# Kernel optimization log

Hardware: AMD Instinct MI355X
Metric: run time of the kernel (lower is better)

## Reference

```python
import jax, jax.numpy as jnp
import numpy as np

N_NODES = 50000
N_REL = 16
N_BASIS = 8
D_IN = 64
D_HID = 64
N_CLASS = 16
N_EDGES = 800000


def setup_inputs() -> dict:
    key = jax.random.key(0)
    ks = jax.random.split(key, 9)
    x = jax.random.normal(ks[0], (N_NODES, D_IN), dtype=jnp.float32)
    edge_index = jax.random.randint(ks[1], (2, N_EDGES), 0, N_NODES, dtype=jnp.int64)
    edge_type = jax.random.randint(ks[2], (N_EDGES,), 0, N_REL, dtype=jnp.int64)
    s1 = 1.0 / np.sqrt(D_IN)
    s2 = 1.0 / np.sqrt(D_HID)
    # layer 1: basis decomposition W_r = sum_b coeffs[r,b] * bases[b]
    bases1 = jax.random.normal(ks[3], (N_BASIS, D_IN, D_HID), dtype=jnp.float32) * s1
    coeffs1 = jax.random.normal(ks[4], (N_REL, N_BASIS), dtype=jnp.float32)
    self1 = jax.random.normal(ks[5], (D_IN, D_HID), dtype=jnp.float32) * s1
    # layer 2
    bases2 = jax.random.normal(ks[6], (N_BASIS, D_HID, N_CLASS), dtype=jnp.float32) * s2
    coeffs2 = jax.random.normal(ks[7], (N_REL, N_BASIS), dtype=jnp.float32)
    self2 = jax.random.normal(ks[8], (D_HID, N_CLASS), dtype=jnp.float32) * s2
    return {"x": x, "bases1": bases1, "coeffs1": coeffs1, "self1": self1,
            "bases2": bases2, "coeffs2": coeffs2, "self2": self2,
            "edge_index": edge_index, "edge_type": edge_type}


def _rgcn_layer(h, bases, coeffs, self_w, src, seg_id, inv_c):
    # normalized messages gathered from source nodes: [E, d]
    msg = h[src] * inv_c[:, None]
    # fused per-(relation, target-node) segment reduce -> [R, N, d]
    agg = jax.ops.segment_sum(msg, seg_id, num_segments=N_REL * N_NODES)
    agg = agg.reshape(N_REL, N_NODES, -1)
    # per-relation weights from basis decomposition: [R, d_in, d_out]
    w_rel = jnp.einsum('rb,bio->rio', coeffs, bases)
    return jnp.einsum('rni,rio->no', agg, w_rel) + h @ self_w


def reference(x, bases1, coeffs1, self1, bases2, coeffs2, self2, edge_index, edge_type):
    src, dst = edge_index[0], edge_index[1]
    # normalization constants: per-relation in-degree of each target node
    counts = jnp.zeros((N_REL, N_NODES), dtype=jnp.float32).at[edge_type, dst].add(1.0)
    inv_c = 1.0 / jnp.maximum(counts[edge_type, dst], 1.0)  # [E]
    seg_id = edge_type * N_NODES + dst  # combined (relation, node) segment key
    h = jax.nn.relu(_rgcn_layer(x, bases1, coeffs1, self1, src, seg_id, inv_c))
    logits = _rgcn_layer(h, bases2, coeffs2, self2, src, seg_id, inv_c)
    return logits
```

## Files before the change

### kernel.cpp

```cpp
#include <hip/hip_runtime.h>

#define N_NODES 50000
#define N_REL 16
#define N_BASIS 8
#define D_IN 64
#define D_HID 64
#define N_CLASS 16
#define N_EDGES 800000
#define N_SBLK 196
#define G1_BLOCKS 782
#define CNT_BLOCKS 3125
#define WREL_BLOCKS 340

typedef short s8v __attribute__((ext_vector_type(8)));
typedef float f4v __attribute__((ext_vector_type(4)));

__device__ inline unsigned short f2bf(float f) {
    union { float f; unsigned u; } v; v.f = f;
    unsigned r = (v.u + 0x7FFFu + ((v.u >> 16) & 1u)) >> 16;
    return (unsigned short)r;
}
__device__ inline float bf2f(unsigned short b) {
    union { unsigned u; float f; } v; v.u = ((unsigned)b) << 16;
    return v.f;
}

__global__ __launch_bounds__(256) void k_pre(const float* __restrict__ b1, const float* __restrict__ c1,
                                             const float* __restrict__ s1f,
                                             const float* __restrict__ b2, const float* __restrict__ c2,
                                             const float* __restrict__ s2f,
                                             unsigned short* __restrict__ w1T,
                                             unsigned short* __restrict__ w2T,
                                             const int* __restrict__ ei,
                                             const int* __restrict__ et,
                                             int* __restrict__ counts) {
    if (blockIdx.x >= WREL_BLOCKS) {
        int e = (blockIdx.x - WREL_BLOCKS) * 256 + threadIdx.x;
        if (e < N_EDGES) {
            int dst = ei[N_EDGES + e];
            int t = et[e];
            atomicAdd(&counts[dst * 16 + t], 1);
        }
        return;
    }
    int idx = blockIdx.x * 256 + threadIdx.x;
    if (idx < 17 * 4096) {
        int r = idx >> 12;
        int o = (idx >> 6) & 63;
        int k = idx & 63;
        float acc = 0.f;
        if (r < 16) {
            #pragma unroll
            for (int b = 0; b < N_BASIS; b++) acc += c1[r * N_BASIS + b] * b1[b * 4096 + k * 64 + o];
        } else {
            acc = s1f[k * 64 + o];
        }
        w1T[idx] = f2bf(acc);
    } else {
        int idx2 = idx - 17 * 4096;
        if (idx2 < 17 * 1024) {
            int r = idx2 >> 10;
            int o = (idx2 >> 6) & 15;
            int k = idx2 & 63;
            float acc = 0.f;
            if (r < 16) {
                #pragma unroll
                for (int b = 0; b < N_BASIS; b++) acc += c2[r * N_BASIS + b] * b2[b * 1024 + k * 16 + o];
            } else {
                acc = s2f[k * 16 + o];
            }
            w2T[idx2] = f2bf(acc);
        }
    }
}

__global__ __launch_bounds__(256) void k_scan_local(const int* __restrict__ counts,
                                                    int* __restrict__ offsets,
                                                    int* __restrict__ bsum) {
    __shared__ int s[256];
    int t = threadIdx.x;
    int i = blockIdx.x * 256 + t;
    int v = 0;
    if (i < N_NODES) {
        const int4* c4 = (const int4*)(counts + i * 16);
        #pragma unroll
        for (int j = 0; j < 4; j++) {
            int4 cv = c4[j];
            v += cv.x + cv.y + cv.z + cv.w;
        }
    }
    s[t] = v;
    __syncthreads();
    #pragma unroll
    for (int off = 1; off < 256; off <<= 1) {
        int x = (t >= off) ? s[t - off] : 0;
        __syncthreads();
        s[t] += x;
        __syncthreads();
    }
    if (i < N_NODES) offsets[i] = s[t] - v;
    if (t == 255) bsum[blockIdx.x] = s[255];
}

__global__ __launch_bounds__(256) void k_scan_bsum(int* __restrict__ bsum) {
    __shared__ int s[256];
    int t = threadIdx.x;
    int v = (t < N_SBLK) ? bsum[t] : 0;
    s[t] = v;
    __syncthreads();
    #pragma unroll
    for (int off = 1; off < 256; off <<= 1) {
        int x = (t >= off) ? s[t - off] : 0;
        __syncthreads();
        s[t] += x;
        __syncthreads();
    }
    if (t < N_SBLK) bsum[t] = s[t] - v;
}

__global__ __launch_bounds__(256) void k_scan_final(int* __restrict__ offsets,
                                                    const int* __restrict__ bsum,
                                                    int* __restrict__ cursor) {
    int i = blockIdx.x * 256 + threadIdx.x;
    if (i < N_NODES) {
        int o = offsets[i] + bsum[blockIdx.x];
        offsets[i] = o;
        cursor[i] = o;
    }
    if (i == 0) offsets[N_NODES] = N_EDGES;
}

__global__ __launch_bounds__(256) void k_fused1(const float* __restrict__ x,
                                                const unsigned short* __restrict__ w1T,
                                                unsigned short* __restrict__ t1,
                                                unsigned short* __restrict__ h,
                                                const int* __restrict__ ei,
                                                const int* __restrict__ et,
                                                const int* __restrict__ counts,
                                                int* __restrict__ cursor,
                                                int2* __restrict__ sed) {
    if (blockIdx.x >= G1_BLOCKS) {
        int e = (blockIdx.x - G1_BLOCKS) * 256 + threadIdx.x;
        if (e < N_EDGES) {
            int src = ei[e];
            int dst = ei[N_EDGES + e];
            int t = et[e];
            int pos = atomicAdd(&cursor[dst], 1);
            float inv = 1.0f / (float)counts[dst * 16 + t];
            sed[pos] = make_int2((t << 16) | src, __float_as_int(inv));
        }
        return;
    }
    __shared__ __align__(16) unsigned short wbuf[2][64 * 64];
    __shared__ __align__(16) unsigned short ou[4][16 * 64];
    int tid = threadIdx.x;
    int wv = tid >> 6, lane = tid & 63;
    int m = lane & 15, q = lane >> 4;
    int nb = blockIdx.x * 64 + wv * 16;
    bool active = (nb < N_NODES);
    int n = active ? (nb + m) : 0;

    const float* xr = x + (size_t)n * 64 + q * 8;
    float4 x0a = *(const float4*)(xr);
    float4 x0b = *(const float4*)(xr + 4);
    float4 x1a = *(const float4*)(xr + 32);
    float4 x1b = *(const float4*)(xr + 36);
    s8v b0, b1;
    b0[0] = f2bf(x0a.x); b0[1] = f2bf(x0a.y); b0[2] = f2bf(x0a.z); b0[3] = f2bf(x0a.w);
    b0[4] = f2bf(x0b.x); b0[5] = f2bf(x0b.y); b0[6] = f2bf(x0b.z); b0[7] = f2bf(x0b.w);
    b1[0] = f2bf(x1a.x); b1[1] = f2bf(x1a.y); b1[2] = f2bf(x1a.z); b1[3] = f2bf(x1a.w);
    b1[4] = f2bf(x1b.x); b1[5] = f2bf(x1b.y); b1[6] = f2bf(x1b.z); b1[7] = f2bf(x1b.w);

    int c0 = tid, c1 = tid + 256;
    int p0s = (c0 >> 3) * 64 + (((c0 & 7) ^ ((c0 >> 3) & 7)) << 3);
    int p1s = (c1 >> 3) * 64 + (((c1 & 7) ^ ((c1 >> 3) & 7)) << 3);

    {
        const int4* src = (const int4*)w1T;
        int4 v0 = src[c0], v1 = src[c1];
        *(int4*)&wbuf[0][p0s] = v0;
        *(int4*)&wbuf[0][p1s] = v1;
    }
    __syncthreads();

    for (int w = 0; w < 17; w++) {
        int cur = w & 1;
        if (w < 16) {
            const int4* src = (const int4*)w1T + (w + 1) * 512;
            int4 v0 = src[c0], v1 = src[c1];
            *(int4*)&wbuf[cur ^ 1][p0s] = v0;
            *(int4*)&wbuf[cur ^ 1][p1s] = v1;
        }
        #pragma unroll
        for (int ct = 0; ct < 4; ct++) {
            int ro = ct * 16 + m;
            int pa = q ^ (ro & 7);
            int pb = (4 + q) ^ (ro & 7);
            s8v A0 = *(const s8v*)&wbuf[cur][ro * 64 + pa * 8];
            s8v A1 = *(const s8v*)&wbuf[cur][ro * 64 + pb * 8];
            f4v acc = (f4v){0.f, 0.f, 0.f, 0.f};
            acc = __builtin_amdgcn_mfma_f32_16x16x32_bf16(A0, b0, acc, 0, 0, 0);
            acc = __builtin_amdgcn_mfma_f32_16x16x32_bf16(A1, b1, acc, 0, 0, 0);
            ushort4 o4;
            o4.x = f2bf(acc[0]); o4.y = f2bf(acc[1]); o4.z = f2bf(acc[2]); o4.w = f2bf(acc[3]);
            int g = ct * 2 + (q >> 1);
            int pg = g ^ (m & 7);
            *(ushort4*)&ou[wv][m * 64 + pg * 8 + (q & 1) * 4] = o4;
        }
        if (active) {
            int r1 = lane >> 3, g1 = lane & 7;
            int pg1 = g1 ^ (r1 & 7);
            int4 d0 = *(const int4*)&ou[wv][r1 * 64 + pg1 * 8];
            int4 d1 = *(const int4*)&ou[wv][(r1 + 8) * 64 + pg1 * 8];
            unsigned short* base = (w < 16) ? (t1 + ((size_t)w * N_NODES + nb) * 64)
                                            : (h + (size_t)nb * 64);
            *(int4*)(base + lane * 8) = d0;
            *(int4*)(base + 512 + lane * 8) = d1;
        }
        __syncthreads();
    }
}

__global__ __launch_bounds__(256) void k_agg1(const int* __restrict__ offsets,
                                              const int2* __restrict__ sed,
                                              const unsigned short* __restrict__ t1,
                                              unsigned short* __restrict__ h) {
    int tid = threadIdx.x;
    int n = blockIdx.x * 4 + (tid >> 6);
    int lane = tid & 63;
    int slot = lane >> 3;
    int d8 = lane & 7;
    int start = offsets[n];
    int end = offsets[n + 1];
    float a[8];
    #pragma unroll
    for (int j = 0; j < 8; j++) a[j] = 0.f;
    for (int i = start + slot; i < end; i += 16) {
        int2 e0 = sed[i];
        bool has1 = (i + 8) < end;
        int2 e1 = has1 ? sed[i + 8] : e0;
        float inv0 = __int_as_float(e0.y);
        float inv1 = has1 ? __int_as_float(e1.y) : 0.f;
        int id0 = e0.x, id1 = e1.x;
        const unsigned short* r0 = t1 + ((size_t)((id0 >> 16) * N_NODES + (id0 & 0xFFFF))) * 64 + d8 * 8;
        const unsigned short* r1 = t1 + ((size_t)((id1 >> 16) * N_NODES + (id1 & 0xFFFF))) * 64 + d8 * 8;
        ushort4 v00 = *(const ushort4*)(r0);
        ushort4 v01 = *(const ushort4*)(r0 + 4);
        ushort4 v10 = *(const ushort4*)(r1);
        ushort4 v11 = *(const ushort4*)(r1 + 4);
        a[0] += inv0 * bf2f(v00.x); a[1] += inv0 * bf2f(v00.y);
        a[2] += inv0 * bf2f(v00.z); a[3] += inv0 * bf2f(v00.w);
        a[4] += inv0 * bf2f(v01.x); a[5] += inv0 * bf2f(v01.y);
        a[6] += inv0 * bf2f(v01.z); a[7] += inv0 * bf2f(v01.w);
        a[0] += inv1 * bf2f(v10.x); a[1] += inv1 * bf2f(v10.y);
        a[2] += inv1 * bf2f(v10.z); a[3] += inv1 * bf2f(v10.w);
        a[4] += inv1 * bf2f(v11.x); a[5] += inv1 * bf2f(v11.y);
        a[6] += inv1 * bf2f(v11.z); a[7] += inv1 * bf2f(v11.w);
    }
    #pragma unroll
    for (int j = 0; j < 8; j++) {
        a[j] += __shfl_xor(a[j], 8, 64);
        a[j] += __shfl_xor(a[j], 16, 64);
        a[j] += __shfl_xor(a[j], 32, 64);
    }
    if (slot == 0) {
        size_t hi = (size_t)n * 64 + d8 * 8;
        ushort4 h0 = *(const ushort4*)(h + hi);
        ushort4 h1 = *(const ushort4*)(h + hi + 4);
        ushort4 o0, o1;
        o0.x = f2bf(bf2f(h0.x) + a[0]); o0.y = f2bf(bf2f(h0.y) + a[1]);
        o0.z = f2bf(bf2f(h0.z) + a[2]); o0.w = f2bf(bf2f(h0.w) + a[3]);
        o1.x = f2bf(bf2f(h1.x) + a[4]); o1.y = f2bf(bf2f(h1.y) + a[5]);
        o1.z = f2bf(bf2f(h1.z) + a[6]); o1.w = f2bf(bf2f(h1.w) + a[7]);
        *(ushort4*)(h + hi) = o0;
        *(ushort4*)(h + hi + 4) = o1;
    }
}

__global__ __launch_bounds__(256) void k_gemm2(const unsigned short* __restrict__ h,
                                               const unsigned short* __restrict__ w2T,
                                               unsigned short* __restrict__ t2, float* __restrict__ out) {
    __shared__ __align__(16) unsigned short wall[272 * 64];
    int tid = threadIdx.x;
    int wv = tid >> 6, lane = tid & 63;
    int m = lane & 15, q = lane >> 4;
    int nb = blockIdx.x * 64 + wv * 16;

    for (int c = tid; c < 2176; c += 256) {
        int4 v = ((const int4*)w2T)[c];
        int row = c >> 3, g = c & 7;
        *(int4*)&wall[row * 64 + ((g ^ (row & 7)) << 3)] = v;
    }
    __syncthreads();
    if (nb >= N_NODES) return;
    int n = nb + m;

    s8v b0 = *(const s8v*)(h + (size_t)n * 64 + q * 8);
    s8v b1 = *(const s8v*)(h + (size_t)n * 64 + 32 + q * 8);
    #pragma unroll
    for (int j = 0; j < 8; j++) {
        if ((unsigned short)b0[j] & 0x8000u) b0[j] = 0;
        if ((unsigned short)b1[j] & 0x8000u) b1[j] = 0;
    }

    for (int w = 0; w < 17; w++) {
        int ro = w * 16 + m;
        int pa = q ^ (ro & 7);
        int pb = (4 + q) ^ (ro & 7);
        s8v A0 = *(const s8v*)&wall[ro * 64 + pa * 8];
        s8v A1 = *(const s8v*)&wall[ro * 64 + pb * 8];
        f4v acc = (f4v){0.f, 0.f, 0.f, 0.f};
        acc = __builtin_amdgcn_mfma_f32_16x16x32_bf16(A0, b0, acc, 0, 0, 0);
        acc = __builtin_amdgcn_mfma_f32_16x16x32_bf16(A1, b1, acc, 0, 0, 0);
        if (w < 16) {
            ushort4 o;
            o.x = f2bf(acc[0]); o.y = f2bf(acc[1]); o.z = f2bf(acc[2]); o.w = f2bf(acc[3]);
            *(ushort4*)(t2 + ((size_t)w * N_NODES + n) * 16 + q * 4) = o;
        } else {
            *(float4*)(out + (size_t)n * 16 + q * 4) = make_float4(acc[0], acc[1], acc[2], acc[3]);
        }
    }
}

__global__ __launch_bounds__(256) void k_agg2(const int* __restrict__ offsets,
                                              const int2* __restrict__ sed,
                                              const unsigned short* __restrict__ t2,
                                              float* __restrict__ out) {
    int tid = threadIdx.x;
    int n = blockIdx.x * 16 + (tid >> 4);
    int sub = tid & 15;
    int slot = sub >> 1;
    int d2 = sub & 1;
    int start = offsets[n];
    int end = offsets[n + 1];
    float a[8];
    #pragma unroll
    for (int j = 0; j < 8; j++) a[j] = 0.f;
    for (int i = start + slot; i < end; i += 16) {
        int2 e0 = sed[i];
        bool has1 = (i + 8) < end;
        int2 e1 = has1 ? sed[i + 8] : e0;
        float inv0 = __int_as_float(e0.y);
        float inv1 = has1 ? __int_as_float(e1.y) : 0.f;
        int id0 = e0.x, id1 = e1.x;
        const unsigned short* r0 = t2 + ((size_t)((id0 >> 16) * N_NODES + (id0 & 0xFFFF))) * 16 + d2 * 8;
        const unsigned short* r1 = t2 + ((size_t)((id1 >> 16) * N_NODES + (id1 & 0xFFFF))) * 16 + d2 * 8;
        ushort4 v00 = *(const ushort4*)(r0);
        ushort4 v01 = *(const ushort4*)(r0 + 4);
        ushort4 v10 = *(const ushort4*)(r1);
        ushort4 v11 = *(const ushort4*)(r1 + 4);
        a[0] += inv0 * bf2f(v00.x); a[1] += inv0 * bf2f(v00.y);
        a[2] += inv0 * bf2f(v00.z); a[3] += inv0 * bf2f(v00.w);
        a[4] += inv0 * bf2f(v01.x); a[5] += inv0 * bf2f(v01.y);
        a[6] += inv0 * bf2f(v01.z); a[7] += inv0 * bf2f(v01.w);
        a[0] += inv1 * bf2f(v10.x); a[1] += inv1 * bf2f(v10.y);
        a[2] += inv1 * bf2f(v10.z); a[3] += inv1 * bf2f(v10.w);
        a[4] += inv1 * bf2f(v11.x); a[5] += inv1 * bf2f(v11.y);
        a[6] += inv1 * bf2f(v11.z); a[7] += inv1 * bf2f(v11.w);
    }
    #pragma unroll
    for (int j = 0; j < 8; j++) {
        a[j] += __shfl_xor(a[j], 2, 64);
        a[j] += __shfl_xor(a[j], 4, 64);
        a[j] += __shfl_xor(a[j], 8, 64);
    }
    if (slot == 0) {
        float* p = out + (size_t)n * 16 + d2 * 8;
        float4 c0 = *(const float4*)p;
        float4 c1 = *(const float4*)(p + 4);
        c0.x += a[0]; c0.y += a[1]; c0.z += a[2]; c0.w += a[3];
        c1.x += a[4]; c1.y += a[5]; c1.z += a[6]; c1.w += a[7];
        *(float4*)p = c0;
        *(float4*)(p + 4) = c1;
    }
}

extern "C" void kernel_launch(void* const* d_in, const int* in_sizes, int n_in,
                              void* d_out, int out_size, void* d_ws, size_t ws_size,
                              hipStream_t stream) {
    const float* x      = (const float*)d_in[0];
    const float* bases1 = (const float*)d_in[1];
    const float* coeffs1= (const float*)d_in[2];
    const float* self1  = (const float*)d_in[3];
    const float* bases2 = (const float*)d_in[4];
    const float* coeffs2= (const float*)d_in[5];
    const float* self2  = (const float*)d_in[6];
    const int*   ei     = (const int*)d_in[7];
    const int*   et     = (const int*)d_in[8];
    float* out = (float*)d_out;

    char* ws = (char*)d_ws;
    int*            counts  = (int*)(ws + 0);
    int*            offsets = (int*)(ws + 3200000);
    int*            cursor  = (int*)(ws + 3400064);
    unsigned short* w1T     = (unsigned short*)(ws + 3600128);
    unsigned short* w2T     = (unsigned short*)(ws + 3739392);
    int*            bsum    = (int*)(ws + 3774208);
    int2*           sed     = (int2*)(ws + 3775232);
    unsigned short* h       = (unsigned short*)(ws + 10175232);
    unsigned short* t1      = (unsigned short*)(ws + 16575232);
    unsigned short* t2      = t1;

    hipMemsetAsync(counts, 0, 3200000, stream);
    k_pre<<<WREL_BLOCKS + CNT_BLOCKS, 256, 0, stream>>>(
        bases1, coeffs1, self1, bases2, coeffs2, self2, w1T, w2T, ei, et, counts);
    k_scan_local<<<N_SBLK, 256, 0, stream>>>(counts, offsets, bsum);
    k_scan_bsum<<<1, 256, 0, stream>>>(bsum);
    k_scan_final<<<N_SBLK, 256, 0, stream>>>(offsets, bsum, cursor);
    k_fused1<<<G1_BLOCKS + CNT_BLOCKS, 256, 0, stream>>>(x, w1T, t1, h, ei, et, counts, cursor, sed);
    k_agg1<<<12500, 256, 0, stream>>>(offsets, sed, t1, h);
    k_gemm2<<<(N_NODES + 63) / 64, 256, 0, stream>>>(h, w2T, t2, out);
    k_agg2<<<3125, 256, 0, stream>>>(offsets, sed, t2, out);
}
```

Before: 222.2 us.

## Fuse layer-1 aggregation with layer-2 GEMM and split GEMM1 across count/scatter kernels

Splits the layer-1 node-transform GEMM into two halves, running one half alongside edge counting and the other alongside the CSR scatter, so both atomic passes overlap tensor work. Layer-1 aggregation is fused with ReLU and the layer-2 MFMA GEMM in one kernel, which removes the intermediate write and reread of h and one launch. Aggregation now uses one lane group per node with 16B loads instead of slot-parallel shuffle reductions. In exchange, each node's edges are walked serially by a single thread, so high-degree nodes can cause load imbalance, and t2 gets its own buffer instead of reusing t1.

```diff
diff --git a/kernel.cpp b/kernel.cpp
--- a/kernel.cpp
+++ b/kernel.cpp
@@ -8,9 +8,8 @@
 #define N_CLASS 16
 #define N_EDGES 800000
 #define N_SBLK 196
-#define G1_BLOCKS 782
+#define G1H_BLOCKS 391
 #define CNT_BLOCKS 3125
-#define WREL_BLOCKS 340
 
 typedef short s8v __attribute__((ext_vector_type(8)));
 typedef float f4v __attribute__((ext_vector_type(4)));
@@ -24,30 +23,26 @@
     union { unsigned u; float f; } v; v.u = ((unsigned)b) << 16;
     return v.f;
 }
-
-__global__ __launch_bounds__(256) void k_pre(const float* __restrict__ b1, const float* __restrict__ c1,
-                                             const float* __restrict__ s1f,
-                                             const float* __restrict__ b2, const float* __restrict__ c2,
-                                             const float* __restrict__ s2f,
-                                             unsigned short* __restrict__ w1T,
-                                             unsigned short* __restrict__ w2T,
-                                             const int* __restrict__ ei,
-                                             const int* __restrict__ et,
-                                             int* __restrict__ counts) {
-    if (blockIdx.x >= WREL_BLOCKS) {
-        int e = (blockIdx.x - WREL_BLOCKS) * 256 + threadIdx.x;
-        if (e < N_EDGES) {
-            int dst = ei[N_EDGES + e];
-            int t = et[e];
-            atomicAdd(&counts[dst * 16 + t], 1);
-        }
-        return;
-    }
+__device__ __forceinline__ void acc8(float* a, float inv, int4 p) {
+    a[0] += inv * __int_as_float((int)((unsigned)p.x << 16));
+    a[1] += inv * __int_as_float(p.x & (int)0xFFFF0000u);
+    a[2] += inv * __int_as_float((int)((unsigned)p.y << 16));
+    a[3] += inv * __int_as_float(p.y & (int)0xFFFF0000u);
+    a[4] += inv * __int_as_float((int)((unsigned)p.z << 16));
+    a[5] += inv * __int_as_float(p.z & (int)0xFFFF0000u);
+    a[6] += inv * __int_as_float((int)((unsigned)p.w << 16));
+    a[7] += inv * __int_as_float(p.w & (int)0xFFFF0000u);
+}
+
+__global__ __launch_bounds__(256) void k_wrel(const float* __restrict__ b1, const float* __restrict__ c1,
+                                              const float* __restrict__ s1f,
+                                              const float* __restrict__ b2, const float* __restrict__ c2,
+                                              const float* __restrict__ s2f,
+                                              unsigned short* __restrict__ w1T,
+                                              unsigned short* __restrict__ w2T) {
     int idx = blockIdx.x * 256 + threadIdx.x;
     if (idx < 17 * 4096) {
-        int r = idx >> 12;
-        int o = (idx >> 6) & 63;
-        int k = idx & 63;
+        int r = idx >> 12, o = (idx >> 6) & 63, k = idx & 63;
         float acc = 0.f;
         if (r < 16) {
             #pragma unroll
@@ -59,9 +54,7 @@
     } else {
         int idx2 = idx - 17 * 4096;
         if (idx2 < 17 * 1024) {
-            int r = idx2 >> 10;
-            int o = (idx2 >> 6) & 15;
-            int k = idx2 & 63;
+            int r = idx2 >> 10, o = (idx2 >> 6) & 15, k = idx2 & 63;
             float acc = 0.f;
             if (r < 16) {
                 #pragma unroll
@@ -72,6 +65,127 @@
             w2T[idx2] = f2bf(acc);
         }
     }
+}
+
+__device__ __forceinline__ void gemm1_tile(int tile, int tid,
+                                           const float* __restrict__ x,
+                                           const unsigned short* __restrict__ w1T,
+                                           unsigned short* __restrict__ t1,
+                                           unsigned short* __restrict__ h,
+                                           unsigned short* wbuf,
+                                           unsigned short* ou) {
+    int wv = tid >> 6, lane = tid & 63;
+    int m = lane & 15, q = lane >> 4;
+    int nb = tile * 64 + wv * 16;
+    bool active = (nb < N_NODES);
+    int n = active ? (nb + m) : 0;
+
+    const float* xr = x + (size_t)n * 64 + q * 8;
+    float4 x0a = *(const float4*)(xr);
+    float4 x0b = *(const float4*)(xr + 4);
+    float4 x1a = *(const float4*)(xr + 32);
+    float4 x1b = *(const float4*)(xr + 36);
+    s8v b0, b1;
+    b0[0] = f2bf(x0a.x); b0[1] = f2bf(x0a.y); b0[2] = f2bf(x0a.z); b0[3] = f2bf(x0a.w);
+    b0[4] = f2bf(x0b.x); b0[5] = f2bf(x0b.y); b0[6] = f2bf(x0b.z); b0[7] = f2bf(x0b.w);
+    b1[0] = f2bf(x1a.x); b1[1] = f2bf(x1a.y); b1[2] = f2bf(x1a.z); b1[3] = f2bf(x1a.w);
+    b1[4] = f2bf(x1b.x); b1[5] = f2bf(x1b.y); b1[6] = f2bf(x1b.z); b1[7] = f2bf(x1b.w);
+
+    int c0 = tid, c1 = tid + 256;
+    int p0s = (c0 >> 3) * 64 + (((c0 & 7) ^ ((c0 >> 3) & 7)) << 3);
+    int p1s = (c1 >> 3) * 64 + (((c1 & 7) ^ ((c1 >> 3) & 7)) << 3);
+
+    {
+        const int4* src = (const int4*)w1T;
+        int4 v0 = src[c0], v1 = src[c1];
+        *(int4*)&wbuf[p0s] = v0;
+        *(int4*)&wbuf[p1s] = v1;
+    }
+    __syncthreads();
+
+    for (int w = 0; w < 17; w++) {
+        int cur = w & 1;
+        if (w < 16) {
+            const int4* src = (const int4*)w1T + (w + 1) * 512;
+            int4 v0 = src[c0], v1 = src[c1];
+            *(int4*)&wbuf[(cur ^ 1) * 4096 + p0s] = v0;
+            *(int4*)&wbuf[(cur ^ 1) * 4096 + p1s] = v1;
+        }
+        #pragma unroll
+        for (int ct = 0; ct < 4; ct++) {
+            int ro = ct * 16 + m;
+            int pa = q ^ (ro & 7);
+            int pb = (4 + q) ^ (ro & 7);
+            s8v A0 = *(const s8v*)&wbuf[cur * 4096 + ro * 64 + pa * 8];
+            s8v A1 = *(const s8v*)&wbuf[cur * 4096 + ro * 64 + pb * 8];
+            f4v acc = (f4v){0.f, 0.f, 0.f, 0.f};
+            acc = __builtin_amdgcn_mfma_f32_16x16x32_bf16(A0, b0, acc, 0, 0, 0);
+            acc = __builtin_amdgcn_mfma_f32_16x16x32_bf16(A1, b1, acc, 0, 0, 0);
+            ushort4 o4;
+            o4.x = f2bf(acc[0]); o4.y = f2bf(acc[1]); o4.z = f2bf(acc[2]); o4.w = f2bf(acc[3]);
+            int g = ct * 2 + (q >> 1);
+            int pg = g ^ (m & 7);
+            *(ushort4*)&ou[wv * 1024 + m * 64 + pg * 8 + (q & 1) * 4] = o4;
+        }
+        if (active) {
+            int r1 = lane >> 3, g1 = lane & 7;
+            int pg1 = g1 ^ (r1 & 7);
+            int4 d0 = *(const int4*)&ou[wv * 1024 + r1 * 64 + pg1 * 8];
+            int4 d1 = *(const int4*)&ou[wv * 1024 + (r1 + 8) * 64 + pg1 * 8];
+            unsigned short* base = (w < 16) ? (t1 + ((size_t)w * N_NODES + nb) * 64)
+                                            : (h + (size_t)nb * 64);
+            *(int4*)(base + lane * 8) = d0;
+            *(int4*)(base + 512 + lane * 8) = d1;
+        }
+        __syncthreads();
+    }
+}
+
+__global__ __launch_bounds__(256) void k_fusedA(const float* __restrict__ x,
+                                                const unsigned short* __restrict__ w1T,
+                                                unsigned short* __restrict__ t1,
+                                                unsigned short* __restrict__ h,
+                                                const int* __restrict__ ei,
+                                                const int* __restrict__ et,
+                                                int* __restrict__ counts) {
+    __shared__ __align__(16) unsigned short wbuf[2 * 4096];
+    __shared__ __align__(16) unsigned short ou[4 * 1024];
+    if (blockIdx.x >= G1H_BLOCKS) {
+        int e = (blockIdx.x - G1H_BLOCKS) * 256 + threadIdx.x;
+        if (e < N_EDGES) {
+            int dst = ei[N_EDGES + e];
+            int t = et[e];
+            atomicAdd(&counts[dst * 16 + t], 1);
+        }
+        return;
+    }
+    gemm1_tile(blockIdx.x, threadIdx.x, x, w1T, t1, h, wbuf, ou);
+}
+
+__global__ __launch_bounds__(256) void k_fusedB(const float* __restrict__ x,
+                                                const unsigned short* __restrict__ w1T,
+                                                unsigned short* __restrict__ t1,
+                                                unsigned short* __restrict__ h,
+                                                const int* __restrict__ ei,
+                                                const int* __restrict__ et,
+                                                const int* __restrict__ counts,
+                                                int* __restrict__ cursor,
+                                                int2* __restrict__ sed) {
+    __shared__ __align__(16) unsigned short wbuf[2 * 4096];
+    __shared__ __align__(16) unsigned short ou[4 * 1024];
+    if (blockIdx.x >= G1H_BLOCKS) {
+        int e = (blockIdx.x - G1H_BLOCKS) * 256 + threadIdx.x;
+        if (e < N_EDGES) {
+            int src = ei[e];
+            int dst = ei[N_EDGES + e];
+            int t = et[e];
+            int pos = atomicAdd(&cursor[dst], 1);
+            float inv = 1.0f / (float)counts[dst * 16 + t];
+            sed[pos] = make_int2((t << 16) | src, __float_as_int(inv));
+        }
+        return;
+    }
+    gemm1_tile(blockIdx.x + G1H_BLOCKS, threadIdx.x, x, w1T, t1, h, wbuf, ou);
 }
 
 __global__ __launch_bounds__(256) void k_scan_local(const int* __restrict__ counts,
@@ -130,194 +244,76 @@
     if (i == 0) offsets[N_NODES] = N_EDGES;
 }
 
-__global__ __launch_bounds__(256) void k_fused1(const float* __restrict__ x,
-                                                const unsigned short* __restrict__ w1T,
-                                                unsigned short* __restrict__ t1,
-                                                unsigned short* __restrict__ h,
-                                                const int* __restrict__ ei,
-                                                const int* __restrict__ et,
-                                                const int* __restrict__ counts,
-                                                int* __restrict__ cursor,
-                                                int2* __restrict__ sed) {
-    if (blockIdx.x >= G1_BLOCKS) {
-        int e = (blockIdx.x - G1_BLOCKS) * 256 + threadIdx.x;
-        if (e < N_EDGES) {
-            int src = ei[e];
-            int dst = ei[N_EDGES + e];
-            int t = et[e];
-            int pos = atomicAdd(&cursor[dst], 1);
-            float inv = 1.0f / (float)counts[dst * 16 + t];
-            sed[pos] = make_int2((t << 16) | src, __float_as_int(inv));
-        }
-        return;
-    }
-    __shared__ __align__(16) unsigned short wbuf[2][64 * 64];
-    __shared__ __align__(16) unsigned short ou[4][16 * 64];
+__global__ __launch_bounds__(256) void k_aggt1(const int* __restrict__ offsets,
+                                               const int2* __restrict__ sed,
+                                               const unsigned short* __restrict__ t1,
+                                               const unsigned short* __restrict__ h,
+                                               const unsigned short* __restrict__ w2T,
+                                               unsigned short* __restrict__ t2,
+                                               float* __restrict__ out) {
     int tid = threadIdx.x;
     int wv = tid >> 6, lane = tid & 63;
     int m = lane & 15, q = lane >> 4;
-    int nb = blockIdx.x * 64 + wv * 16;
-    bool active = (nb < N_NODES);
-    int n = active ? (nb + m) : 0;
-
-    const float* xr = x + (size_t)n * 64 + q * 8;
-    float4 x0a = *(const float4*)(xr);
-    float4 x0b = *(const float4*)(xr + 4);
-    float4 x1a = *(const float4*)(xr + 32);
-    float4 x1b = *(const float4*)(xr + 36);
-    s8v b0, b1;
-    b0[0] = f2bf(x0a.x); b0[1] = f2bf(x0a.y); b0[2] = f2bf(x0a.z); b0[3] = f2bf(x0a.w);
-    b0[4] = f2bf(x0b.x); b0[5] = f2bf(x0b.y); b0[6] = f2bf(x0b.z); b0[7] = f2bf(x0b.w);
-    b1[0] = f2bf(x1a.x); b1[1] = f2bf(x1a.y); b1[2] = f2bf(x1a.z); b1[3] = f2bf(x1a.w);
-    b1[4] = f2bf(x1b.x); b1[5] = f2bf(x1b.y); b1[6] = f2bf(x1b.z); b1[7] = f2bf(x1b.w);
-
-    int c0 = tid, c1 = tid + 256;
-    int p0s = (c0 >> 3) * 64 + (((c0 & 7) ^ ((c0 >> 3) & 7)) << 3);
-    int p1s = (c1 >> 3) * 64 + (((c1 & 7) ^ ((c1 >> 3) & 7)) << 3);
-
-    {
-        const int4* src = (const int4*)w1T;
-        int4 v0 = src[c0], v1 = src[c1];
-        *(int4*)&wbuf[0][p0s] = v0;
-        *(int4*)&wbuf[0][p1s] = v1;
-    }
-    __syncthreads();
-
-    for (int w = 0; w < 17; w++) {
-        int cur = w & 1;
-        if (w < 16) {
-            const int4* src = (const int4*)w1T + (w + 1) * 512;
-            int4 v0 = src[c0], v1 = src[c1];
-            *(int4*)&wbuf[cur ^ 1][p0s] = v0;
-            *(int4*)&wbuf[cur ^ 1][p1s] = v1;
-        }
-        #pragma unroll
-        for (int ct = 0; ct < 4; ct++) {
-            int ro = ct * 16 + m;
-            int pa = q ^ (ro & 7);
-            int pb = (4 + q) ^ (ro & 7);
-            s8v A0 = *(const s8v*)&wbuf[cur][ro * 64 + pa * 8];
-            s8v A1 = *(const s8v*)&wbuf[cur][ro * 64 + pb * 8];
-            f4v acc = (f4v){0.f, 0.f, 0.f, 0.f};
-            acc = __builtin_amdgcn_mfma_f32_16x16x32_bf16(A0, b0, acc, 0, 0, 0);
-            acc = __builtin_amdgcn_mfma_f32_16x16x32_bf16(A1, b1, acc, 0, 0, 0);
-            ushort4 o4;
-            o4.x = f2bf(acc[0]); o4.y = f2bf(acc[1]); o4.z = f2bf(acc[2]); o4.w = f2bf(acc[3]);
-            int g = ct * 2 + (q >> 1);
-            int pg = g ^ (m & 7);
-            *(ushort4*)&ou[wv][m * 64 + pg * 8 + (q & 1) * 4] = o4;
-        }
-        if (active) {
-            int r1 = lane >> 3, g1 = lane & 7;
-            int pg1 = g1 ^ (r1 & 7);
-            int4 d0 = *(const int4*)&ou[wv][r1 * 64 + pg1 * 8];
-            int4 d1 = *(const int4*)&ou[wv][(r1 + 8) * 64 + pg1 * 8];
-            unsigned short* base = (w < 16) ? (t1 + ((size_t)w * N_NODES + nb) * 64)
-                                            : (h + (size_t)nb * 64);
-            *(int4*)(base + lane * 8) = d0;
-            *(int4*)(base + 512 + lane * 8) = d1;
-        }
-        __syncthreads();
-    }
-}
-
-__global__ __launch_bounds__(256) void k_agg1(const int* __restrict__ offsets,
-                                              const int2* __restrict__ sed,
-                                              const unsigned short* __restrict__ t1,
-                                              unsigned short* __restrict__ h) {
-    int tid = threadIdx.x;
-    int n = blockIdx.x * 4 + (tid >> 6);
-    int lane = tid & 63;
-    int slot = lane >> 3;
-    int d8 = lane & 7;
-    int start = offsets[n];
-    int end = offsets[n + 1];
-    float a[8];
+    int nb16 = blockIdx.x * 64 + wv * 16;
+    if (nb16 >= N_NODES) return;
+    int n = nb16 + m;
+    bool act = (n < N_NODES);
+    int s = act ? offsets[n] : 0;
+    int e = act ? offsets[n + 1] : 0;
+
+    float a0[8], a1[8];
     #pragma unroll
-    for (int j = 0; j < 8; j++) a[j] = 0.f;
-    for (int i = start + slot; i < end; i += 16) {
+    for (int j = 0; j < 8; j++) { a0[j] = 0.f; a1[j] = 0.f; }
+
+    for (int i = s; i < e; i += 2) {
         int2 e0 = sed[i];
-        bool has1 = (i + 8) < end;
-        int2 e1 = has1 ? sed[i + 8] : e0;
+        bool has1 = (i + 1) < e;
+        int2 e1 = has1 ? sed[i + 1] : e0;
         float inv0 = __int_as_float(e0.y);
         float inv1 = has1 ? __int_as_float(e1.y) : 0.f;
-        int id0 = e0.x, id1 = e1.x;
-        const unsigned short* r0 = t1 + ((size_t)((id0 >> 16) * N_NODES + (id0 & 0xFFFF))) * 64 + d8 * 8;
-        const unsigned short* r1 = t1 + ((size_t)((id1 >> 16) * N_NODES + (id1 & 0xFFFF))) * 64 + d8 * 8;
-        ushort4 v00 = *(const ushort4*)(r0);
-        ushort4 v01 = *(const ushort4*)(r0 + 4);
-        ushort4 v10 = *(const ushort4*)(r1);
-        ushort4 v11 = *(const ushort4*)(r1 + 4);
-        a[0] += inv0 * bf2f(v00.x); a[1] += inv0 * bf2f(v00.y);
-        a[2] += inv0 * bf2f(v00.z); a[3] += inv0 * bf2f(v00.w);
-        a[4] += inv0 * bf2f(v01.x); a[5] += inv0 * bf2f(v01.y);
-        a[6] += inv0 * bf2f(v01.z); a[7] += inv0 * bf2f(v01.w);
-        a[0] += inv1 * bf2f(v10.x); a[1] += inv1 * bf2f(v10.y);
-        a[2] += inv1 * bf2f(v10.z); a[3] += inv1 * bf2f(v10.w);
-        a[4] += inv1 * bf2f(v11.x); a[5] += inv1 * bf2f(v11.y);
-        a[6] += inv1 * bf2f(v11.z); a[7] += inv1 * bf2f(v11.w);
-    }
+        const unsigned short* r0 =
+            t1 + ((size_t)(((unsigned)e0.x >> 16) * N_NODES + (e0.x & 0xFFFF))) * 64;
+        const unsigned short* r1 =
+            t1 + ((size_t)(((unsigned)e1.x >> 16) * N_NODES + (e1.x & 0xFFFF))) * 64;
+        int4 p00 = *(const int4*)(r0 + q * 8);
+        int4 p01 = *(const int4*)(r0 + 32 + q * 8);
+        int4 p10 = *(const int4*)(r1 + q * 8);
+        int4 p11 = *(const int4*)(r1 + 32 + q * 8);
+        acc8(a0, inv0, p00);
+        acc8(a1, inv0, p01);
+        acc8(a0, inv1, p10);
+        acc8(a1, inv1, p11);
+    }
+    if (act) {
+        int4 hs0 = *(const int4*)(h + (size_t)n * 64 + q * 8);
+        int4 hs1 = *(const int4*)(h + (size_t)n * 64 + 32 + q * 8);
+        acc8(a0, 1.0f, hs0);
+        acc8(a1, 1.0f, hs1);
+    }
+    s8v b0, b1;
     #pragma unroll
     for (int j = 0; j < 8; j++) {
-        a[j] += __shfl_xor(a[j], 8, 64);
-        a[j] += __shfl_xor(a[j], 16, 64);
-        a[j] += __shfl_xor(a[j], 32, 64);
-    }
-    if (slot == 0) {
-        size_t hi = (size_t)n * 64 + d8 * 8;
-        ushort4 h0 = *(const ushort4*)(h + hi);
-        ushort4 h1 = *(const ushort4*)(h + hi + 4);
-        ushort4 o0, o1;
-        o0.x = f2bf(bf2f(h0.x) + a[0]); o0.y = f2bf(bf2f(h0.y) + a[1]);
-        o0.z = f2bf(bf2f(h0.z) + a[2]); o0.w = f2bf(bf2f(h0.w) + a[3]);
-        o1.x = f2bf(bf2f(h1.x) + a[4]); o1.y = f2bf(bf2f(h1.y) + a[5]);
-        o1.z = f2bf(bf2f(h1.z) + a[6]); o1.w = f2bf(bf2f(h1.w) + a[7]);
-        *(ushort4*)(h + hi) = o0;
-        *(ushort4*)(h + hi + 4) = o1;
-    }
-}
-
-__global__ __launch_bounds__(256) void k_gemm2(const unsigned short* __restrict__ h,
-                                               const unsigned short* __restrict__ w2T,
-                                               unsigned short* __restrict__ t2, float* __restrict__ out) {
-    __shared__ __align__(16) unsigned short wall[272 * 64];
-    int tid = threadIdx.x;
-    int wv = tid >> 6, lane = tid & 63;
-    int m = lane & 15, q = lane >> 4;
-    int nb = blockIdx.x * 64 + wv * 16;
-
-    for (int c = tid; c < 2176; c += 256) {
-        int4 v = ((const int4*)w2T)[c];
-        int row = c >> 3, g = c & 7;
-        *(int4*)&wall[row * 64 + ((g ^ (row & 7)) << 3)] = v;
-    }
-    __syncthreads();
-    if (nb >= N_NODES) return;
-    int n = nb + m;
-
-    s8v b0 = *(const s8v*)(h + (size_t)n * 64 + q * 8);
-    s8v b1 = *(const s8v*)(h + (size_t)n * 64 + 32 + q * 8);
-    #pragma unroll
-    for (int j = 0; j < 8; j++) {
-        if ((unsigned short)b0[j] & 0x8000u) b0[j] = 0;
-        if ((unsigned short)b1[j] & 0x8000u) b1[j] = 0;
-    }
-
+        float v0 = a0[j] > 0.f ? a0[j] : 0.f;
+        float v1 = a1[j] > 0.f ? a1[j] : 0.f;
+        b0[j] = (short)f2bf(v0);
+        b1[j] = (short)f2bf(v1);
+    }
+
+    const unsigned short* wp = w2T + m * 64 + q * 8;
     for (int w = 0; w < 17; w++) {
-        int ro = w * 16 + m;
-        int pa = q ^ (ro & 7);
-        int pb = (4 + q) ^ (ro & 7);
-        s8v A0 = *(const s8v*)&wall[ro * 64 + pa * 8];
-        s8v A1 = *(const s8v*)&wall[ro * 64 + pb * 8];
+        s8v A0 = *(const s8v*)(wp + (w << 10));
+        s8v A1 = *(const s8v*)(wp + (w << 10) + 32);
         f4v acc = (f4v){0.f, 0.f, 0.f, 0.f};
         acc = __builtin_amdgcn_mfma_f32_16x16x32_bf16(A0, b0, acc, 0, 0, 0);
         acc = __builtin_amdgcn_mfma_f32_16x16x32_bf16(A1, b1, acc, 0, 0, 0);
-        if (w < 16) {
-            ushort4 o;
-            o.x = f2bf(acc[0]); o.y = f2bf(acc[1]); o.z = f2bf(acc[2]); o.w = f2bf(acc[3]);
-            *(ushort4*)(t2 + ((size_t)w * N_NODES + n) * 16 + q * 4) = o;
-        } else {
-            *(float4*)(out + (size_t)n * 16 + q * 4) = make_float4(acc[0], acc[1], acc[2], acc[3]);
+        if (act) {
+            if (w < 16) {
+                ushort4 o;
+                o.x = f2bf(acc[0]); o.y = f2bf(acc[1]); o.z = f2bf(acc[2]); o.w = f2bf(acc[3]);
+                *(ushort4*)(t2 + ((size_t)w * N_NODES + n) * 16 + q * 4) = o;
+            } else {
+                *(float4*)(out + (size_t)n * 16 + q * 4) = make_float4(acc[0], acc[1], acc[2], acc[3]);
+            }
         }
     }
 }
@@ -327,51 +323,38 @@
                                               const unsigned short* __restrict__ t2,
                                               float* __restrict__ out) {
     int tid = threadIdx.x;
-    int n = blockIdx.x * 16 + (tid >> 4);
-    int sub = tid & 15;
-    int slot = sub >> 1;
-    int d2 = sub & 1;
-    int start = offsets[n];
-    int end = offsets[n + 1];
-    float a[8];
-    #pragma unroll
-    for (int j = 0; j < 8; j++) a[j] = 0.f;
-    for (int i = start + slot; i < end; i += 16) {
+    int wv = tid >> 6, lane = tid & 63;
+    int m = lane & 15, q = lane >> 4;
+    int nb16 = blockIdx.x * 64 + wv * 16;
+    if (nb16 >= N_NODES) return;
+    int n = nb16 + m;
+    bool act = (n < N_NODES);
+    int s = act ? offsets[n] : 0;
+    int e = act ? offsets[n + 1] : 0;
+
+    float a[4] = {0.f, 0.f, 0.f, 0.f};
+    for (int i = s; i < e; i += 2) {
         int2 e0 = sed[i];
-        bool has1 = (i + 8) < end;
-        int2 e1 = has1 ? sed[i + 8] : e0;
+        bool has1 = (i + 1) < e;
+        int2 e1 = has1 ? sed[i + 1] : e0;
         float inv0 = __int_as_float(e0.y);
         float inv1 = has1 ? __int_as_float(e1.y) : 0.f;
-        int id0 = e0.x, id1 = e1.x;
-        const unsigned short* r0 = t2 + ((size_t)((id0 >> 16) * N_NODES + (id0 & 0xFFFF))) * 16 + d2 * 8;
-        const unsigned short* r1 = t2 + ((size_t)((id1 >> 16) * N_NODES + (id1 & 0xFFFF))) * 16 + d2 * 8;
-        ushort4 v00 = *(const ushort4*)(r0);
-        ushort4 v01 = *(const ushort4*)(r0 + 4);
-        ushort4 v10 = *(const ushort4*)(r1);
-        ushort4 v11 = *(const ushort4*)(r1 + 4);
-        a[0] += inv0 * bf2f(v00.x); a[1] += inv0 * bf2f(v00.y);
-        a[2] += inv0 * bf2f(v00.z); a[3] += inv0 * bf2f(v00.w);
-        a[4] += inv0 * bf2f(v01.x); a[5] += inv0 * bf2f(v01.y);
-        a[6] += inv0 * bf2f(v01.z); a[7] += inv0 * bf2f(v01.w);
-        a[0] += inv1 * bf2f(v10.x); a[1] += inv1 * bf2f(v10.y);
-        a[2] += inv1 * bf2f(v10.z); a[3] += inv1 * bf2f(v10.w);
-        a[4] += inv1 * bf2f(v11.x); a[5] += inv1 * bf2f(v11.y);
-        a[6] += inv1 * bf2f(v11.z); a[7] += inv1 * bf2f(v11.w);
-    }
-    #pragma unroll
-    for (int j = 0; j < 8; j++) {
-        a[j] += __shfl_xor(a[j], 2, 64);
-        a[j] += __shfl_xor(a[j], 4, 64);
-        a[j] += __shfl_xor(a[j], 8, 64);
-    }
-    if (slot == 0) {
-        float* p = out + (size_t)n * 16 + d2 * 8;
-        float4 c0 = *(const float4*)p;
-        float4 c1 = *(const float4*)(p + 4);
-        c0.x += a[0]; c0.y += a[1]; c0.z += a[2]; c0.w += a[3];
-        c1.x += a[4]; c1.y += a[5]; c1.z += a[6]; c1.w += a[7];
-        *(float4*)p = c0;
-        *(float4*)(p + 4) = c1;
+        const unsigned short* r0 =
+            t2 + ((size_t)(((unsigned)e0.x >> 16) * N_NODES + (e0.x & 0xFFFF))) * 16 + q * 4;
+        const unsigned short* r1 =
+            t2 + ((size_t)(((unsigned)e1.x >> 16) * N_NODES + (e1.x & 0xFFFF))) * 16 + q * 4;
+        ushort4 v0 = *(const ushort4*)(r0);
+        ushort4 v1 = *(const ushort4*)(r1);
+        a[0] += inv0 * bf2f(v0.x) + inv1 * bf2f(v1.x);
+        a[1] += inv0 * bf2f(v0.y) + inv1 * bf2f(v1.y);
+        a[2] += inv0 * bf2f(v0.z) + inv1 * bf2f(v1.z);
+        a[3] += inv0 * bf2f(v0.w) + inv1 * bf2f(v1.w);
+    }
+    if (act) {
+        float* p = out + (size_t)n * 16 + q * 4;
+        float4 c = *(const float4*)p;
+        c.x += a[0]; c.y += a[1]; c.z += a[2]; c.w += a[3];
+        *(float4*)p = c;
     }
 }
 
@@ -399,16 +382,16 @@
     int2*           sed     = (int2*)(ws + 3775232);
     unsigned short* h       = (unsigned short*)(ws + 10175232);
     unsigned short* t1      = (unsigned short*)(ws + 16575232);
-    unsigned short* t2      = t1;
+    unsigned short* t2      = (unsigned short*)(ws + 118975232);
 
     hipMemsetAsync(counts, 0, 3200000, stream);
-    k_pre<<<WREL_BLOCKS + CNT_BLOCKS, 256, 0, stream>>>(
-        bases1, coeffs1, self1, bases2, coeffs2, self2, w1T, w2T, ei, et, counts);
+    k_wrel<<<(17 * 4096 + 17 * 1024 + 255) / 256, 256, 0, stream>>>(
+        bases1, coeffs1, self1, bases2, coeffs2, self2, w1T, w2T);
+    k_fusedA<<<G1H_BLOCKS + CNT_BLOCKS, 256, 0, stream>>>(x, w1T, t1, h, ei, et, counts);
     k_scan_local<<<N_SBLK, 256, 0, stream>>>(counts, offsets, bsum);
     k_scan_bsum<<<1, 256, 0, stream>>>(bsum);
     k_scan_final<<<N_SBLK, 256, 0, stream>>>(offsets, bsum, cursor);
-    k_fused1<<<G1_BLOCKS + CNT_BLOCKS, 256, 0, stream>>>(x, w1T, t1, h, ei, et, counts, cursor, sed);
-    k_agg1<<<12500, 256, 0, stream>>>(offsets, sed, t1, h);
-    k_gemm2<<<(N_NODES + 63) / 64, 256, 0, stream>>>(h, w2T, t2, out);
-    k_agg2<<<3125, 256, 0, stream>>>(offsets, sed, t2, out);
-}
+    k_fusedB<<<G1H_BLOCKS + CNT_BLOCKS, 256, 0, stream>>>(x, w1T, t1, h, ei, et, counts, cursor, sed);
+    k_aggt1<<<782, 256, 0, stream>>>(offsets, sed, t1, h, w2T, t2, out);
+    k_agg2<<<782, 256, 0, stream>>>(offsets, sed, t2, out);
+}
```

New measurement: 249.1 us. 12.1% more time.
